# Kernel optimization log

Measured on AMD Instinct MI355X. Metric: run time of the kernel, lower is better.

## Reference

```python
import jax, jax.numpy as jnp
import numpy as np

NUM_USERS = 100000
NUM_ITEMS = 50000
N_NODES = NUM_USERS + NUM_ITEMS
EMBED_DIM = 64
N_LAYERS = 3
NNZ = 4000000


def setup_inputs() -> dict:
    key = jax.random.key(0)
    k1, k2, k3, k4, k5 = jax.random.split(key, 5)
    # Xavier-uniform-ish embedding tables (exact init distribution irrelevant for correctness)
    user_emb = jax.random.normal(k1, (NUM_USERS, EMBED_DIM), dtype=jnp.float32) * 0.1
    item_emb = jax.random.normal(k2, (NUM_ITEMS, EMBED_DIM), dtype=jnp.float32) * 0.1
    # Sparse normalized adjacency in COO form; scale values like a degree-normalized graph
    vals = jax.random.uniform(k3, (NNZ,), dtype=jnp.float32) * 0.02
    rows = jax.random.randint(k4, (NNZ,), 0, N_NODES, dtype=jnp.int32)
    cols = jax.random.randint(k5, (NNZ,), 0, N_NODES, dtype=jnp.int32)
    return {"user_emb": user_emb, "item_emb": item_emb, "vals": vals,
            "rows": rows, "cols": cols}


def _spmm(vals, rows, cols, x):
    # out[r] = sum_{e: rows[e]==r} vals[e] * x[cols[e]]  -- COO SpMM
    return jax.ops.segment_sum(vals[:, None] * x[cols], rows, num_segments=N_NODES)


def reference(user_emb, item_emb, vals, rows, cols):
    all_emb = jnp.concatenate([user_emb, item_emb], axis=0)  # [N, D]
    emb_sum = all_emb
    h = all_emb
    for _ in range(N_LAYERS):
        h = _spmm(vals, rows, cols, h)
        emb_sum = emb_sum + h
    final = emb_sum / jnp.float32(N_LAYERS + 1)  # mean over layer stack
    users = final[:NUM_USERS]
    items = final[NUM_USERS:]
    return users, items
```

## Files before the change

### kernel.cpp

```cpp
#include <hip/hip_runtime.h>
#include <hip/hip_bf16.h>


#define NUSERS 100000
#define NITEMS 50000
#define NNODES 150000
#define DIM    64
#define NNZ_E  4000000
#define BSH    9
#define NBKT   ((NNODES + 511) / 512)
#define CHUNK  8192
#define NB1    ((NNZ_E + CHUNK - 1) / CHUNK)

__device__ inline unsigned short f2b(float f) {
    __hip_bfloat16 h = __float2bfloat16(f);
    return *reinterpret_cast<unsigned short*>(&h);
}
__device__ inline float b2f(unsigned short b) {
    return __uint_as_float((unsigned)b << 16);
}


__global__ void bhist_k(const int* __restrict__ rows, int* __restrict__ bcnt) {
    __shared__ int cnt[NBKT];
    for (int i = threadIdx.x; i < NBKT; i += 256) cnt[i] = 0;
    __syncthreads();
    int stride = gridDim.x * 256;
    for (int i = blockIdx.x * 256 + threadIdx.x; i < NNZ_E; i += stride)
        atomicAdd(&cnt[rows[i] >> BSH], 1);
    __syncthreads();
    for (int i = threadIdx.x; i < NBKT; i += 256)
        if (cnt[i]) atomicAdd(&bcnt[i], cnt[i]);
}


__global__ void bscan_k(const int* __restrict__ bcnt, int* __restrict__ bbase,
                        int* __restrict__ bcur, int* __restrict__ rs) {
    __shared__ int s[512];
    int t = threadIdx.x;
    int v = (t < NBKT) ? bcnt[t] : 0;
    s[t] = v;
    __syncthreads();
    for (int off = 1; off < 512; off <<= 1) {
        int add = (t >= off) ? s[t - off] : 0;
        __syncthreads();
        s[t] += add;
        __syncthreads();
    }
    if (t < NBKT) {
        int ex = s[t] - v;
        bbase[t] = ex;
        bcur[t]  = ex;
    }
    if (t == 0) {
        bbase[NBKT] = NNZ_E;
        rs[NNODES]  = NNZ_E;
    }
}


__global__ void pass1_k(const int* __restrict__ rows, const int* __restrict__ cols,
                        const float* __restrict__ vals, int* __restrict__ bcur,
                        int2* __restrict__ ebuf) {
    __shared__ int lcnt[NBKT];
    __shared__ int lcur[NBKT];
    int base = blockIdx.x * CHUNK;
    int end  = min(base + CHUNK, NNZ_E);
    for (int i = threadIdx.x; i < NBKT; i += 256) lcnt[i] = 0;
    __syncthreads();
    for (int i = base + threadIdx.x; i < end; i += 256)
        atomicAdd(&lcnt[rows[i] >> BSH], 1);
    __syncthreads();
    for (int i = threadIdx.x; i < NBKT; i += 256)
        lcur[i] = lcnt[i] ? atomicAdd(&bcur[i], lcnt[i]) : 0;
    __syncthreads();
    for (int i = base + threadIdx.x; i < end; i += 256) {
        int r = rows[i];
        int p = atomicAdd(&lcur[r >> BSH], 1);
        ebuf[p] = make_int2(cols[i] | ((r & 511) << 18), __float_as_int(vals[i]));
    }
}


__global__ void passC_k(const int* __restrict__ bbase, const int2* __restrict__ ebuf,
                        int* __restrict__ rs, int2* __restrict__ cedge) {
    __shared__ int rcnt[512];
    __shared__ int rbase[512];
    __shared__ int s[256];
    int b  = blockIdx.x;
    int t  = threadIdx.x;
    int s0 = bbase[b], e0 = bbase[b + 1];
    int rows0 = b << BSH;
    int nrows = min(512, NNODES - rows0);

    rcnt[t] = 0; rcnt[t + 256] = 0;
    __syncthreads();
    for (int j = s0 + t; j < e0; j += 256)
        atomicAdd(&rcnt[(unsigned)ebuf[j].x >> 18], 1);
    __syncthreads();

    int a0 = rcnt[2 * t], a1 = rcnt[2 * t + 1];
    s[t] = a0 + a1;
    __syncthreads();
    for (int off = 1; off < 256; off <<= 1) {
        int add = (t >= off) ? s[t - off] : 0;
        __syncthreads();
        s[t] += add;
        __syncthreads();
    }
    int pbase = s[t] - (a0 + a1);
    rbase[2 * t]     = pbase;
    rbase[2 * t + 1] = pbase + a0;
    __syncthreads();

    if (t < nrows)           rs[rows0 + t]       = s0 + rbase[t];
    if (t + 256 < nrows)     rs[rows0 + t + 256] = s0 + rbase[t + 256];

    rcnt[t] = rbase[t]; rcnt[t + 256] = rbase[t + 256];
    __syncthreads();

    for (int j = s0 + t; j < e0; j += 256) {
        int2 ee = ebuf[j];
        int lr  = (unsigned)ee.x >> 18;
        int pos = s0 + atomicAdd(&rcnt[lr], 1);
        cedge[pos] = make_int2(ee.x & 0x3FFFF, ee.y);
    }
}


__global__ void init_k(const float4* __restrict__ ue, const float4* __restrict__ ie,
                       ushort4* __restrict__ h0, float4* __restrict__ esum) {
    int i = blockIdx.x * 256 + threadIdx.x;
    const int NU4 = NUSERS * (DIM / 4);
    const int NT4 = NNODES * (DIM / 4);
    if (i < NT4) {
        float4 v = (i < NU4) ? ue[i] : ie[i - NU4];
        esum[i] = v;
        ushort4 b;
        b.x = f2b(v.x); b.y = f2b(v.y); b.z = f2b(v.z); b.w = f2b(v.w);
        h0[i] = b;
    }
}


template <int FINAL>
__global__ void spmm_k(const int* __restrict__ rs, const int2* __restrict__ cedge,
                       const unsigned short* __restrict__ x,
                       unsigned short* __restrict__ hout, float* __restrict__ esum) {
    int w    = (blockIdx.x * blockDim.x + threadIdx.x) >> 6;
    int lane = threadIdx.x & 63;
    if (w >= NNODES) return;
    int s = rs[w], e = rs[w + 1];
    float acc = 0.f;
    int j = s;
    for (; j + 8 <= e; j += 8) {
        int2 e0 = cedge[j],     e1 = cedge[j + 1];
        int2 e2 = cedge[j + 2], e3 = cedge[j + 3];
        int2 e4 = cedge[j + 4], e5 = cedge[j + 5];
        int2 e6 = cedge[j + 6], e7 = cedge[j + 7];
        float x0 = b2f(x[e0.x * DIM + lane]);
        float x1 = b2f(x[e1.x * DIM + lane]);
        float x2 = b2f(x[e2.x * DIM + lane]);
        float x3 = b2f(x[e3.x * DIM + lane]);
        float x4 = b2f(x[e4.x * DIM + lane]);
        float x5 = b2f(x[e5.x * DIM + lane]);
        float x6 = b2f(x[e6.x * DIM + lane]);
        float x7 = b2f(x[e7.x * DIM + lane]);
        acc = fmaf(__int_as_float(e0.y), x0, acc);
        acc = fmaf(__int_as_float(e1.y), x1, acc);
        acc = fmaf(__int_as_float(e2.y), x2, acc);
        acc = fmaf(__int_as_float(e3.y), x3, acc);
        acc = fmaf(__int_as_float(e4.y), x4, acc);
        acc = fmaf(__int_as_float(e5.y), x5, acc);
        acc = fmaf(__int_as_float(e6.y), x6, acc);
        acc = fmaf(__int_as_float(e7.y), x7, acc);
    }
    for (; j < e; ++j) {
        int2 ee = cedge[j];
        acc = fmaf(__int_as_float(ee.y), b2f(x[ee.x * DIM + lane]), acc);
    }

    int o = w * DIM + lane;
    float r = esum[o] + acc;
    if (FINAL) {
        esum[o] = r * 0.25f;
    } else {
        esum[o] = r;
        hout[o] = f2b(acc);
    }
}


extern "C" void kernel_launch(void* const* d_in, const int* in_sizes, int n_in,
                              void* d_out, int out_size, void* d_ws, size_t ws_size,
                              hipStream_t stream) {
    const float* ue   = (const float*)d_in[0];
    const float* ie   = (const float*)d_in[1];
    const float* vals = (const float*)d_in[2];
    const int*   rows = (const int*)d_in[3];
    const int*   cols = (const int*)d_in[4];
    float*       out  = (float*)d_out;

    char*  ws  = (char*)d_ws;
    size_t off = 0;
    auto alloc = [&](size_t bytes) -> char* {
        char* p = ws + off;
        off += (bytes + 255) & ~size_t(255);
        return p;
    };
    unsigned short* h0 = (unsigned short*)alloc((size_t)NNODES * DIM * 2);
    unsigned short* h1 = (unsigned short*)alloc((size_t)NNODES * DIM * 2);
    int2*  cedge  = (int2*)alloc((size_t)NNZ_E * 8);
    int2*  ebuf   = (int2*)alloc((size_t)NNZ_E * 8);
    int*   rs     = (int*)alloc((size_t)(NNODES + 1) * 4);
    int*   bcnt   = (int*)alloc((size_t)(NBKT + 1) * 4);
    int*   bbase  = (int*)alloc((size_t)(NBKT + 1) * 4);
    int*   bcur   = (int*)alloc((size_t)(NBKT + 1) * 4);
    (void)in_sizes; (void)n_in; (void)out_size;

    if (ws_size < off) return;

    hipMemsetAsync(bcnt, 0, (size_t)(NBKT + 1) * 4, stream);
    bhist_k<<<256, 256, 0, stream>>>(rows, bcnt);
    bscan_k<<<1, 512, 0, stream>>>(bcnt, bbase, bcur, rs);
    pass1_k<<<NB1, 256, 0, stream>>>(rows, cols, vals, bcur, ebuf);
    passC_k<<<NBKT, 256, 0, stream>>>(bbase, ebuf, rs, cedge);

    init_k<<<(NNODES * (DIM / 4) + 255) / 256, 256, 0, stream>>>(
        (const float4*)ue, (const float4*)ie, (ushort4*)h0, (float4*)out);

    const int SG = (NNODES * 64) / 256;
    spmm_k<0><<<SG, 256, 0, stream>>>(rs, cedge, h0, h1, out);
    spmm_k<0><<<SG, 256, 0, stream>>>(rs, cedge, h1, h0, out);
    spmm_k<1><<<SG, 256, 0, stream>>>(rs, cedge, h0, h1, out);
}
```

Baseline: 678.5 us.

## Process two rows per wavefront with 32-bit packed bf16 gathers in SpMM

Each 64-lane wavefront now handles two rows, 32 lanes per row. Each lane loads one 32-bit word holding two bf16 features and keeps two accumulators. Global loads per edge become wider and half as many wavefronts are launched, which should cut instruction count and improve memory request efficiency on the gather. The cost is that the two halves of a wavefront may have different row lengths, so lanes can diverge.

```diff
diff --git a/kernel.cpp b/kernel.cpp
--- a/kernel.cpp
+++ b/kernel.cpp
@@ -147,46 +147,67 @@
 __global__ void spmm_k(const int* __restrict__ rs, const int2* __restrict__ cedge,
                        const unsigned short* __restrict__ x,
                        unsigned short* __restrict__ hout, float* __restrict__ esum) {
-    int w    = (blockIdx.x * blockDim.x + threadIdx.x) >> 6;
+    int pair = (blockIdx.x * blockDim.x + threadIdx.x) >> 6;
     int lane = threadIdx.x & 63;
-    if (w >= NNODES) return;
-    int s = rs[w], e = rs[w + 1];
-    float acc = 0.f;
+    int half = lane >> 5;
+    int m    = lane & 31;
+    int row  = pair * 2 + half;
+    if (row >= NNODES) return;
+    int s = rs[row], e = rs[row + 1];
+    const char* xb = (const char*)x;
+
+    float acc0 = 0.f, acc1 = 0.f;
     int j = s;
     for (; j + 8 <= e; j += 8) {
         int2 e0 = cedge[j],     e1 = cedge[j + 1];
         int2 e2 = cedge[j + 2], e3 = cedge[j + 3];
         int2 e4 = cedge[j + 4], e5 = cedge[j + 5];
         int2 e6 = cedge[j + 6], e7 = cedge[j + 7];
-        float x0 = b2f(x[e0.x * DIM + lane]);
-        float x1 = b2f(x[e1.x * DIM + lane]);
-        float x2 = b2f(x[e2.x * DIM + lane]);
-        float x3 = b2f(x[e3.x * DIM + lane]);
-        float x4 = b2f(x[e4.x * DIM + lane]);
-        float x5 = b2f(x[e5.x * DIM + lane]);
-        float x6 = b2f(x[e6.x * DIM + lane]);
-        float x7 = b2f(x[e7.x * DIM + lane]);
-        acc = fmaf(__int_as_float(e0.y), x0, acc);
-        acc = fmaf(__int_as_float(e1.y), x1, acc);
-        acc = fmaf(__int_as_float(e2.y), x2, acc);
-        acc = fmaf(__int_as_float(e3.y), x3, acc);
-        acc = fmaf(__int_as_float(e4.y), x4, acc);
-        acc = fmaf(__int_as_float(e5.y), x5, acc);
-        acc = fmaf(__int_as_float(e6.y), x6, acc);
-        acc = fmaf(__int_as_float(e7.y), x7, acc);
+        unsigned u0 = *(const unsigned*)(xb + ((size_t)e0.x << 7) + (m << 2));
+        unsigned u1 = *(const unsigned*)(xb + ((size_t)e1.x << 7) + (m << 2));
+        unsigned u2 = *(const unsigned*)(xb + ((size_t)e2.x << 7) + (m << 2));
+        unsigned u3 = *(const unsigned*)(xb + ((size_t)e3.x << 7) + (m << 2));
+        unsigned u4 = *(const unsigned*)(xb + ((size_t)e4.x << 7) + (m << 2));
+        unsigned u5 = *(const unsigned*)(xb + ((size_t)e5.x << 7) + (m << 2));
+        unsigned u6 = *(const unsigned*)(xb + ((size_t)e6.x << 7) + (m << 2));
+        unsigned u7 = *(const unsigned*)(xb + ((size_t)e7.x << 7) + (m << 2));
+        float v0 = __int_as_float(e0.y), v1 = __int_as_float(e1.y);
+        float v2 = __int_as_float(e2.y), v3 = __int_as_float(e3.y);
+        float v4 = __int_as_float(e4.y), v5 = __int_as_float(e5.y);
+        float v6 = __int_as_float(e6.y), v7 = __int_as_float(e7.y);
+        acc0 = fmaf(v0, __uint_as_float(u0 << 16), acc0);
+        acc1 = fmaf(v0, __uint_as_float(u0 & 0xffff0000u), acc1);
+        acc0 = fmaf(v1, __uint_as_float(u1 << 16), acc0);
+        acc1 = fmaf(v1, __uint_as_float(u1 & 0xffff0000u), acc1);
+        acc0 = fmaf(v2, __uint_as_float(u2 << 16), acc0);
+        acc1 = fmaf(v2, __uint_as_float(u2 & 0xffff0000u), acc1);
+        acc0 = fmaf(v3, __uint_as_float(u3 << 16), acc0);
+        acc1 = fmaf(v3, __uint_as_float(u3 & 0xffff0000u), acc1);
+        acc0 = fmaf(v4, __uint_as_float(u4 << 16), acc0);
+        acc1 = fmaf(v4, __uint_as_float(u4 & 0xffff0000u), acc1);
+        acc0 = fmaf(v5, __uint_as_float(u5 << 16), acc0);
+        acc1 = fmaf(v5, __uint_as_float(u5 & 0xffff0000u), acc1);
+        acc0 = fmaf(v6, __uint_as_float(u6 << 16), acc0);
+        acc1 = fmaf(v6, __uint_as_float(u6 & 0xffff0000u), acc1);
+        acc0 = fmaf(v7, __uint_as_float(u7 << 16), acc0);
+        acc1 = fmaf(v7, __uint_as_float(u7 & 0xffff0000u), acc1);
     }
     for (; j < e; ++j) {
         int2 ee = cedge[j];
-        acc = fmaf(__int_as_float(ee.y), b2f(x[ee.x * DIM + lane]), acc);
-    }
-
-    int o = w * DIM + lane;
-    float r = esum[o] + acc;
+        unsigned u = *(const unsigned*)(xb + ((size_t)ee.x << 7) + (m << 2));
+        float v = __int_as_float(ee.y);
+        acc0 = fmaf(v, __uint_as_float(u << 16), acc0);
+        acc1 = fmaf(v, __uint_as_float(u & 0xffff0000u), acc1);
+    }
+
+    int o2 = row * 32 + m;
+    float2 rv = ((const float2*)esum)[o2];
+    float r0 = rv.x + acc0, r1 = rv.y + acc1;
     if (FINAL) {
-        esum[o] = r * 0.25f;
+        ((float2*)esum)[o2] = make_float2(r0 * 0.25f, r1 * 0.25f);
     } else {
-        esum[o] = r;
-        hout[o] = f2b(acc);
+        ((float2*)esum)[o2] = make_float2(r0, r1);
+        ((unsigned*)hout)[o2] = ((unsigned)f2b(acc1) << 16) | f2b(acc0);
     }
 }
 
@@ -229,7 +250,7 @@
     init_k<<<(NNODES * (DIM / 4) + 255) / 256, 256, 0, stream>>>(
         (const float4*)ue, (const float4*)ie, (ushort4*)h0, (float4*)out);
 
-    const int SG = (NNODES * 64) / 256;
+    const int SG = (NNODES / 2) * 64 / 256;
     spmm_k<0><<<SG, 256, 0, stream>>>(rs, cedge, h0, h1, out);
     spmm_k<0><<<SG, 256, 0, stream>>>(rs, cedge, h1, h0, out);
     spmm_k<1><<<SG, 256, 0, stream>>>(rs, cedge, h0, h1, out);
```

New measurement: 554.8 us. 18.2% less time.
